# Optimization experiments

Hardware: AMD Instinct MI355X
Metric: run time of the kernel (lower is better)

Reference implementation:

```python
import jax, jax.numpy as jnp
import numpy as np
from jax.scipy.linalg import expm

DELTA = 0.01  # time step from __init__ delta
B_SZ, U_DIM, DU_DIM, H_DIM, Y_DIM = 512, 1024, 512, 2048, 1024


def setup_inputs() -> dict:
    key = jax.random.key(0)
    ks = jax.random.split(key, 6)
    inv_sqrt = lambda fan_in: 1.0 / np.sqrt(fan_in)
    u = jax.random.normal(ks[0], (B_SZ, U_DIM), jnp.float32)
    du = jax.random.normal(ks[1], (B_SZ, DU_DIM), jnp.float32)
    # torch.nn.Linear default init: U(-1/sqrt(fan_in), 1/sqrt(fan_in))
    W = jax.random.uniform(ks[2], (H_DIM, H_DIM), jnp.float32, -inv_sqrt(H_DIM), inv_sqrt(H_DIM))
    Bw = jax.random.uniform(ks[3], (H_DIM, U_DIM + DU_DIM), jnp.float32, -inv_sqrt(U_DIM + DU_DIM), inv_sqrt(U_DIM + DU_DIM))
    Cw = jax.random.uniform(ks[4], (Y_DIM, H_DIM), jnp.float32, -inv_sqrt(H_DIM), inv_sqrt(H_DIM))
    h = jax.random.normal(ks[5], (1, H_DIM), jnp.float32)
    return {"u": u, "du": du, "W": W, "Bw": Bw, "Cw": Cw, "h": h}


def reference(u, du, W, Bw, Cw, h):
    # Antisymmetric part of W
    A = 0.5 * (W - W.T)                                    # (H,H)
    A_expm = expm(A * DELTA)                               # (H,H) matrix exponential
    rec = h @ A_expm.T                                     # (1,H) recurrent term: F.linear(h, A_expm)
    A_inv = jnp.linalg.inv(A)                              # (H,H)
    # B(cat([du, u])) : (B, H)
    b = jnp.concatenate([du, u], axis=1) @ Bw.T
    # M = A^{-1} (expm(A*delta) - I); input term = M @ b^T per sample -> b @ M^T
    M = A_inv @ (A_expm - jnp.eye(H_DIM, dtype=A.dtype))   # (H,H)
    inp = b @ M.T                                          # (B,H)
    h_new = rec + inp                                      # broadcast (1,H)+(B,H) -> (B,H)
    y = h_new @ Cw.T                                       # (B,Y)
    return y
```

## Files before the change

### kernel.cpp

```cpp
#include <hip/hip_runtime.h>
#include <hip/hip_bf16.h>


#define B_SZ 512
#define U_DIM 1024
#define DU_DIM 512
#define H_DIM 2048
#define Y_DIM 1024
#define K_CAT 1536
#define DELTA_F 0.01f

typedef __hip_bfloat16 bf16;
using bf16x8f = __attribute__((ext_vector_type(8))) short;
using f32x4   = __attribute__((ext_vector_type(4))) float;

__device__ __forceinline__ short f2bs(float x) {
  union { bf16 b; short s; } u; u.b = __float2bfloat16(x); return u.s;
}
__device__ __forceinline__ int4 pack8(const float4 v0, const float4 v1) {
  union { short s[8]; int4 i; } o;
  o.s[0] = f2bs(v0.x); o.s[1] = f2bs(v0.y); o.s[2] = f2bs(v0.z); o.s[3] = f2bs(v0.w);
  o.s[4] = f2bs(v1.x); o.s[5] = f2bs(v1.y); o.s[6] = f2bs(v1.z); o.s[7] = f2bs(v1.w);
  return o.i;
}

#define LDP 72
#define LDS_SHORTS (2 * 32 * LDP + 2 * 64 * LDP)

#define NB (H_DIM * K_CAT / 8)

__global__ __launch_bounds__(256) void k1(const float* __restrict__ W, const float* __restrict__ h,
                                          const float* __restrict__ Bw, float* __restrict__ wh,
                                          float* __restrict__ wtp, short* __restrict__ Bwb) {
  const int b = blockIdx.x;
  if (b < 512) {
    const int lane = threadIdx.x & 63, wave = threadIdx.x >> 6;
    const int row = b * 4 + wave;
    const float* wr = W + (size_t)row * H_DIM;
    float s = 0.f;
#pragma unroll
    for (int it = 0; it < 8; it++) {
      int k = it * 256 + lane * 4;
      float4 a = *(const float4*)(wr + k);
      float4 hv = *(const float4*)(h + k);
      s += a.x * hv.x + a.y * hv.y + a.z * hv.z + a.w * hv.w;
    }
#pragma unroll
    for (int off = 32; off > 0; off >>= 1) s += __shfl_down(s, off);
    if (lane == 0) wh[row] = s;
  } else if (b < 768) {
    const int e = b - 512;
    const int colg = e & 7, rowg = e >> 3;
    const int k = colg * 256 + threadIdx.x;
    float s = 0.f;
    const float* base = W + (size_t)rowg * 64 * H_DIM + k;
#pragma unroll 8
    for (int i = 0; i < 64; i++) s += base[(size_t)i * H_DIM] * h[rowg * 64 + i];
    wtp[rowg * H_DIM + k] = s;
  } else {
    for (int g = (b - 768) * 256 + threadIdx.x; g < NB; g += 256 * 256) {
      int e = g * 8;
      *(int4*)(Bwb + e) = pack8(*(const float4*)(Bw + e), *(const float4*)(Bw + e + 4));
    }
  }
}

__device__ __forceinline__ void k2_tile(short* lds, float* recf, const float* __restrict__ du,
                                        const float* __restrict__ u, const short* __restrict__ B,
                                        const float* __restrict__ h, const float* __restrict__ wh,
                                        const float* __restrict__ wtp, short* __restrict__ out,
                                        int mt, int nt) {
  const int KDIM = K_CAT;
  short* As0 = lds;
  short* Bs0 = lds + 2 * 32 * LDP;
  const int tid = threadIdx.x;
  const int lane = tid & 63, wave = tid >> 6;
  const int wm = wave >> 1, wn = wave & 1;
  const int row0 = mt * 32, col0 = nt * 64;
  const int rA = tid >> 3, kc = (tid & 7) * 8;
  f32x4 acc[2] = {};
  int4 pa, pb1, pb2;
  auto ldA = [&](int kt) -> int4 {
    int col = kt * 64 + kc;
    const float* p = (col < DU_DIM) ? du + (size_t)(row0 + rA) * DU_DIM + col
                                    : u + (size_t)(row0 + rA) * U_DIM + (col - DU_DIM);
    return pack8(*(const float4*)p, *(const float4*)(p + 4));
  };
  auto ldB1 = [&](int kt) { return *(const int4*)(B + (size_t)(col0 + rA) * KDIM + kt * 64 + kc); };
  auto ldB2 = [&](int kt) { return *(const int4*)(B + (size_t)(col0 + rA + 32) * KDIM + kt * 64 + kc); };
  pa = ldA(0); pb1 = ldB1(0); pb2 = ldB2(0);
  *(int4*)&As0[rA * LDP + kc] = pa;
  *(int4*)&Bs0[rA * LDP + kc] = pb1;
  *(int4*)&Bs0[(rA + 32) * LDP + kc] = pb2;
  const int NT = KDIM / 64;
  const int kq = (lane >> 4) * 8, rm = lane & 15;
  for (int kt = 0; kt < NT; kt++) {
    const int cur = kt & 1;
    if (kt + 1 < NT) { pa = ldA(kt + 1); pb1 = ldB1(kt + 1); pb2 = ldB2(kt + 1); }
    __syncthreads();
    const short* Ac = As0 + cur * (32 * LDP);
    const short* Bc = Bs0 + cur * (64 * LDP);
    bf16x8f af[2], bfr[2][2];
#pragma unroll
    for (int ks = 0; ks < 2; ks++) {
      af[ks] = *(const bf16x8f*)&Ac[(wm * 16 + rm) * LDP + ks * 32 + kq];
#pragma unroll
      for (int j = 0; j < 2; j++)
        bfr[ks][j] = *(const bf16x8f*)&Bc[(wn * 32 + 16 * j + rm) * LDP + ks * 32 + kq];
    }
#pragma unroll
    for (int ks = 0; ks < 2; ks++)
#pragma unroll
      for (int j = 0; j < 2; j++)
        acc[j] = __builtin_amdgcn_mfma_f32_16x16x32_bf16(af[ks], bfr[ks][j], acc[j], 0, 0, 0);
    if (kt + 1 < NT) {
      short* An = As0 + (cur ^ 1) * (32 * LDP);
      short* Bn = Bs0 + (cur ^ 1) * (64 * LDP);
      *(int4*)&An[rA * LDP + kc] = pa;
      *(int4*)&Bn[rA * LDP + kc] = pb1;
      *(int4*)&Bn[(rA + 32) * LDP + kc] = pb2;
      __syncthreads();
    }
  }
  if (tid < 64) {
    int gc = col0 + tid;
    float s = 0.f;
#pragma unroll
    for (int p = 0; p < 32; p++) s += wtp[p * H_DIM + gc];
    recf[tid] = h[gc] + 0.005f * (wh[gc] - s);
  }
  __syncthreads();
  const int quad = lane >> 4;
#pragma unroll
  for (int j = 0; j < 2; j++) {
    int gc = col0 + wn * 32 + 16 * j + rm;
#pragma unroll
    for (int r = 0; r < 4; r++) {
      int gr = row0 + wm * 16 + quad * 4 + r;
      out[(size_t)gr * H_DIM + gc] = f2bs(recf[gc - col0] + DELTA_F * acc[j][r]);
    }
  }
}

__global__ __launch_bounds__(256) void k2(const float* __restrict__ du, const float* __restrict__ u,
                                          const short* __restrict__ Bwb, const float* __restrict__ h,
                                          const float* __restrict__ wh, const float* __restrict__ wtp,
                                          short* __restrict__ bb, const float* __restrict__ Cw,
                                          short* __restrict__ Cwb) {
  __shared__ __align__(16) short lds[LDS_SHORTS];
  __shared__ float recf[64];
  const int b = blockIdx.x;
  if (b < 512) {
    k2_tile(lds, recf, du, u, Bwb, h, wh, wtp, bb, b >> 5, b & 31);
  } else {
    int g = (b - 512) * 256 + threadIdx.x;
    int e = g * 8;
    *(int4*)(Cwb + e) = pack8(*(const float4*)(Cw + e), *(const float4*)(Cw + e + 4));
    e = (g + 131072) * 8;
    *(int4*)(Cwb + e) = pack8(*(const float4*)(Cw + e), *(const float4*)(Cw + e + 4));
  }
}

__global__ __launch_bounds__(256) void k3(const short* __restrict__ A, const short* __restrict__ B,
                                          float* __restrict__ y) {
  __shared__ __align__(16) short lds[LDS_SHORTS];
  const int KDIM = H_DIM;
  short* As0 = lds;
  short* Bs0 = lds + 2 * 32 * LDP;
  const int tid = threadIdx.x;
  const int lane = tid & 63, wave = tid >> 6;
  const int wm = wave >> 1, wn = wave & 1;
  const int mt = blockIdx.x >> 5, nt = blockIdx.x & 31;
  const int row0 = mt * 32, col0 = nt * 32;
  const int rA = tid >> 3, kc = (tid & 7) * 8;
  f32x4 acc = {};
  int4 pa, pb;
  auto ldA = [&](int kt) { return *(const int4*)(A + (size_t)(row0 + rA) * KDIM + kt * 64 + kc); };
  auto ldB = [&](int kt) { return *(const int4*)(B + (size_t)(col0 + rA) * KDIM + kt * 64 + kc); };
  pa = ldA(0); pb = ldB(0);
  *(int4*)&As0[rA * LDP + kc] = pa;
  *(int4*)&Bs0[rA * LDP + kc] = pb;
  const int NT = KDIM / 64;
  const int kq = (lane >> 4) * 8, rm = lane & 15;
  for (int kt = 0; kt < NT; kt++) {
    const int cur = kt & 1;
    if (kt + 1 < NT) { pa = ldA(kt + 1); pb = ldB(kt + 1); }
    __syncthreads();
    const short* Ac = As0 + cur * (32 * LDP);
    const short* Bc = Bs0 + cur * (32 * LDP);
#pragma unroll
    for (int ks = 0; ks < 2; ks++) {
      bf16x8f af = *(const bf16x8f*)&Ac[(wm * 16 + rm) * LDP + ks * 32 + kq];
      bf16x8f bf = *(const bf16x8f*)&Bc[(wn * 16 + rm) * LDP + ks * 32 + kq];
      acc = __builtin_amdgcn_mfma_f32_16x16x32_bf16(af, bf, acc, 0, 0, 0);
    }
    if (kt + 1 < NT) {
      short* An = As0 + (cur ^ 1) * (32 * LDP);
      short* Bn = Bs0 + (cur ^ 1) * (32 * LDP);
      *(int4*)&An[rA * LDP + kc] = pa;
      *(int4*)&Bn[rA * LDP + kc] = pb;
      __syncthreads();
    }
  }
  const int quad = lane >> 4;
  int gc = col0 + wn * 16 + rm;
#pragma unroll
  for (int r = 0; r < 4; r++) {
    int gr = row0 + wm * 16 + quad * 4 + r;
    y[(size_t)gr * Y_DIM + gc] = acc[r];
  }
}

extern "C" void kernel_launch(void* const* d_in, const int* in_sizes, int n_in,
                              void* d_out, int out_size, void* d_ws, size_t ws_size,
                              hipStream_t stream) {
  const float* u  = (const float*)d_in[0];
  const float* du = (const float*)d_in[1];
  const float* W  = (const float*)d_in[2];
  const float* Bw = (const float*)d_in[3];
  const float* Cw = (const float*)d_in[4];
  const float* h  = (const float*)d_in[5];
  float* y = (float*)d_out;

  char* w = (char*)d_ws;
  size_t off = 0;
  short* Bwb = (short*)(w + off); off += (size_t)H_DIM * K_CAT * sizeof(short);
  short* Cwb = (short*)(w + off); off += (size_t)Y_DIM * H_DIM * sizeof(short);
  short* bb  = (short*)(w + off); off += (size_t)B_SZ * H_DIM * sizeof(short);
  float* wh  = (float*)(w + off); off += H_DIM * sizeof(float);
  float* wtp = (float*)(w + off); off += 32 * H_DIM * sizeof(float);
  if (ws_size < off) return;

  k1<<<1024, 256, 0, stream>>>(W, h, Bw, wh, wtp, Bwb);
  k2<<<1024, 256, 0, stream>>>(du, u, Bwb, h, wh, wtp, bb, Cw, Cwb);
  k3<<<512, 256, 0, stream>>>(bb, Cwb, y);
}
```

Baseline: 122.1 us.

## Fuse second and third GEMM kernels with per-row-tile atomic flag barriers

Moves the Cw bf16 conversion into the first kernel alongside the Bw conversion and rebalances its block split. Fuses the b-projection GEMM and the output GEMM into one persistent-style kernel. Each block signals a per-row-tile counter and spins until all 32 column tiles of its 32-row slice are written, then computes its output tile. This removes one kernel launch and the global drain between the stages. In exchange it depends on all 512 blocks being co-resident (guarded by an occupancy query) and adds spin-wait and fence overhead.

```diff
diff --git a/kernel.cpp b/kernel.cpp
--- a/kernel.cpp
+++ b/kernel.cpp
@@ -26,44 +26,6 @@
 
 #define LDP 72
 #define LDS_SHORTS (2 * 32 * LDP + 2 * 64 * LDP)
-
-#define NB (H_DIM * K_CAT / 8)
-
-__global__ __launch_bounds__(256) void k1(const float* __restrict__ W, const float* __restrict__ h,
-                                          const float* __restrict__ Bw, float* __restrict__ wh,
-                                          float* __restrict__ wtp, short* __restrict__ Bwb) {
-  const int b = blockIdx.x;
-  if (b < 512) {
-    const int lane = threadIdx.x & 63, wave = threadIdx.x >> 6;
-    const int row = b * 4 + wave;
-    const float* wr = W + (size_t)row * H_DIM;
-    float s = 0.f;
-#pragma unroll
-    for (int it = 0; it < 8; it++) {
-      int k = it * 256 + lane * 4;
-      float4 a = *(const float4*)(wr + k);
-      float4 hv = *(const float4*)(h + k);
-      s += a.x * hv.x + a.y * hv.y + a.z * hv.z + a.w * hv.w;
-    }
-#pragma unroll
-    for (int off = 32; off > 0; off >>= 1) s += __shfl_down(s, off);
-    if (lane == 0) wh[row] = s;
-  } else if (b < 768) {
-    const int e = b - 512;
-    const int colg = e & 7, rowg = e >> 3;
-    const int k = colg * 256 + threadIdx.x;
-    float s = 0.f;
-    const float* base = W + (size_t)rowg * 64 * H_DIM + k;
-#pragma unroll 8
-    for (int i = 0; i < 64; i++) s += base[(size_t)i * H_DIM] * h[rowg * 64 + i];
-    wtp[rowg * H_DIM + k] = s;
-  } else {
-    for (int g = (b - 768) * 256 + threadIdx.x; g < NB; g += 256 * 256) {
-      int e = g * 8;
-      *(int4*)(Bwb + e) = pack8(*(const float4*)(Bw + e), *(const float4*)(Bw + e + 4));
-    }
-  }
-}
 
 __device__ __forceinline__ void k2_tile(short* lds, float* recf, const float* __restrict__ du,
                                         const float* __restrict__ u, const short* __restrict__ B,
@@ -142,35 +104,15 @@
   }
 }
 
-__global__ __launch_bounds__(256) void k2(const float* __restrict__ du, const float* __restrict__ u,
-                                          const short* __restrict__ Bwb, const float* __restrict__ h,
-                                          const float* __restrict__ wh, const float* __restrict__ wtp,
-                                          short* __restrict__ bb, const float* __restrict__ Cw,
-                                          short* __restrict__ Cwb) {
-  __shared__ __align__(16) short lds[LDS_SHORTS];
-  __shared__ float recf[64];
-  const int b = blockIdx.x;
-  if (b < 512) {
-    k2_tile(lds, recf, du, u, Bwb, h, wh, wtp, bb, b >> 5, b & 31);
-  } else {
-    int g = (b - 512) * 256 + threadIdx.x;
-    int e = g * 8;
-    *(int4*)(Cwb + e) = pack8(*(const float4*)(Cw + e), *(const float4*)(Cw + e + 4));
-    e = (g + 131072) * 8;
-    *(int4*)(Cwb + e) = pack8(*(const float4*)(Cw + e), *(const float4*)(Cw + e + 4));
-  }
-}
-
-__global__ __launch_bounds__(256) void k3(const short* __restrict__ A, const short* __restrict__ B,
-                                          float* __restrict__ y) {
-  __shared__ __align__(16) short lds[LDS_SHORTS];
+__device__ __forceinline__ void k3_tile(short* lds, const short* __restrict__ A,
+                                        const short* __restrict__ B, float* __restrict__ y,
+                                        int mt, int nt) {
   const int KDIM = H_DIM;
   short* As0 = lds;
   short* Bs0 = lds + 2 * 32 * LDP;
   const int tid = threadIdx.x;
   const int lane = tid & 63, wave = tid >> 6;
   const int wm = wave >> 1, wn = wave & 1;
-  const int mt = blockIdx.x >> 5, nt = blockIdx.x & 31;
   const int row0 = mt * 32, col0 = nt * 32;
   const int rA = tid >> 3, kc = (tid & 7) * 8;
   f32x4 acc = {};
@@ -211,6 +153,88 @@
   }
 }
 
+#define NB (H_DIM * K_CAT / 8)
+#define NC (Y_DIM * H_DIM / 8)
+
+__global__ __launch_bounds__(256) void k1(const float* __restrict__ W, const float* __restrict__ h,
+                                          const float* __restrict__ Bw, const float* __restrict__ Cw,
+                                          float* __restrict__ wh, float* __restrict__ wtp,
+                                          short* __restrict__ Bwb, short* __restrict__ Cwb,
+                                          int* __restrict__ flags) {
+  const int b = blockIdx.x;
+  if (b == 0 && threadIdx.x < 16) flags[threadIdx.x] = 0;
+  if (b < 256) {
+    const int lane = threadIdx.x & 63, wave = threadIdx.x >> 6;
+#pragma unroll
+    for (int i = 0; i < 2; i++) {
+      const int row = b * 8 + wave * 2 + i;
+      const float* wr = W + (size_t)row * H_DIM;
+      float s = 0.f;
+#pragma unroll
+      for (int it = 0; it < 8; it++) {
+        int k = it * 256 + lane * 4;
+        float4 a = *(const float4*)(wr + k);
+        float4 hv = *(const float4*)(h + k);
+        s += a.x * hv.x + a.y * hv.y + a.z * hv.z + a.w * hv.w;
+      }
+#pragma unroll
+      for (int off = 32; off > 0; off >>= 1) s += __shfl_down(s, off);
+      if (lane == 0) wh[row] = s;
+    }
+  } else if (b < 512) {
+    const int e = b - 256;
+    const int colg = e & 7, rowg = e >> 3;
+    const int k = colg * 256 + threadIdx.x;
+    float s = 0.f;
+    const float* base = W + (size_t)rowg * 64 * H_DIM + k;
+#pragma unroll 8
+    for (int i = 0; i < 64; i++) s += base[(size_t)i * H_DIM] * h[rowg * 64 + i];
+    wtp[rowg * H_DIM + k] = s;
+  } else {
+    for (int g = (b - 512) * 256 + threadIdx.x; g < NB + NC; g += 512 * 256) {
+      const float* src; short* dst;
+      if (g < NB) { int e = g * 8; src = Bw + e; dst = Bwb + e; }
+      else        { int e = (g - NB) * 8; src = Cw + e; dst = Cwb + e; }
+      *(int4*)dst = pack8(*(const float4*)src, *(const float4*)(src + 4));
+    }
+  }
+}
+
+__global__ void k23_fused(const float* __restrict__ du, const float* __restrict__ u,
+                          const short* __restrict__ Bwb, const float* __restrict__ h,
+                          const float* __restrict__ wh, const float* __restrict__ wtp,
+                          short* __restrict__ bb, const short* __restrict__ Cwb,
+                          float* __restrict__ y, int* __restrict__ flags) {
+  __shared__ __align__(16) short lds[LDS_SHORTS];
+  __shared__ float recf[64];
+  const int mt = blockIdx.x >> 5, nt = blockIdx.x & 31;
+  k2_tile(lds, recf, du, u, Bwb, h, wh, wtp, bb, mt, nt);
+  __threadfence();
+  __syncthreads();
+  if (threadIdx.x == 0) {
+    __hip_atomic_fetch_add(&flags[mt], 1, __ATOMIC_RELEASE, __HIP_MEMORY_SCOPE_AGENT);
+    while (__hip_atomic_load(&flags[mt], __ATOMIC_ACQUIRE, __HIP_MEMORY_SCOPE_AGENT) < 32)
+      __builtin_amdgcn_s_sleep(2);
+  }
+  __syncthreads();
+  __threadfence();
+  k3_tile(lds, bb, Cwb, y, mt, nt);
+}
+
+__global__ __launch_bounds__(256) void k2_plain(const float* __restrict__ du, const float* __restrict__ u,
+                                                const short* __restrict__ Bwb, const float* __restrict__ h,
+                                                const float* __restrict__ wh, const float* __restrict__ wtp,
+                                                short* __restrict__ bb) {
+  __shared__ __align__(16) short lds[LDS_SHORTS];
+  __shared__ float recf[64];
+  k2_tile(lds, recf, du, u, Bwb, h, wh, wtp, bb, blockIdx.x >> 5, blockIdx.x & 31);
+}
+__global__ __launch_bounds__(256) void k3_plain(const short* __restrict__ bb, const short* __restrict__ Cwb,
+                                                float* __restrict__ y) {
+  __shared__ __align__(16) short lds[LDS_SHORTS];
+  k3_tile(lds, bb, Cwb, y, blockIdx.x >> 5, blockIdx.x & 31);
+}
+
 extern "C" void kernel_launch(void* const* d_in, const int* in_sizes, int n_in,
                               void* d_out, int out_size, void* d_ws, size_t ws_size,
                               hipStream_t stream) {
@@ -229,9 +253,18 @@
   short* bb  = (short*)(w + off); off += (size_t)B_SZ * H_DIM * sizeof(short);
   float* wh  = (float*)(w + off); off += H_DIM * sizeof(float);
   float* wtp = (float*)(w + off); off += 32 * H_DIM * sizeof(float);
+  int* flags = (int*)(w + off);   off += 16 * sizeof(int);
   if (ws_size < off) return;
 
-  k1<<<1024, 256, 0, stream>>>(W, h, Bw, wh, wtp, Bwb);
-  k2<<<1024, 256, 0, stream>>>(du, u, Bwb, h, wh, wtp, bb, Cw, Cwb);
-  k3<<<512, 256, 0, stream>>>(bb, Cwb, y);
-}
+  k1<<<1024, 256, 0, stream>>>(W, h, Bw, Cw, wh, wtp, Bwb, Cwb, flags);
+
+  int occ = 0;
+  hipError_t e = hipOccupancyMaxActiveBlocksPerMultiprocessor(
+      &occ, reinterpret_cast<const void*>(&k23_fused), 256, 0);
+  if (e == hipSuccess && occ >= 2) {
+    k23_fused<<<512, 256, 0, stream>>>(du, u, Bwb, h, wh, wtp, bb, Cwb, y, flags);
+  } else {
+    k2_plain<<<512, 256, 0, stream>>>(du, u, Bwb, h, wh, wtp, bb);
+    k3_plain<<<512, 256, 0, stream>>>(bb, Cwb, y);
+  }
+}
```

Measured after the change: 232.8 us. +90.7%, slower.

## Convert weights to bf16 inside GEMM loads and split recurrent term into a rank-1 bias

Applied to the files above, without the earlier changes.

Drops the separate passes that write bf16 copies of Bw and Cw; each GEMM now reads the fp32 weights and converts them as it loads tiles. The recurrent term is no longer added to bb before the second GEMM. A small kernel computes Cw·rec once per output column, and that vector is added in the final GEMM epilogue, so bb only holds the scaled input term. The W·h reductions are interleaved with the first GEMM tiles in one launch. In exchange, the GEMMs read twice the weight bytes in fp32, and each tile converts its weights again instead of once up front.

```diff
diff --git a/kernel.cpp b/kernel.cpp
--- a/kernel.cpp
+++ b/kernel.cpp
@@ -27,49 +27,9 @@
 #define LDP 72
 #define LDS_SHORTS (2 * 32 * LDP + 2 * 64 * LDP)
 
-#define NB (H_DIM * K_CAT / 8)
-
-__global__ __launch_bounds__(256) void k1(const float* __restrict__ W, const float* __restrict__ h,
-                                          const float* __restrict__ Bw, float* __restrict__ wh,
-                                          float* __restrict__ wtp, short* __restrict__ Bwb) {
-  const int b = blockIdx.x;
-  if (b < 512) {
-    const int lane = threadIdx.x & 63, wave = threadIdx.x >> 6;
-    const int row = b * 4 + wave;
-    const float* wr = W + (size_t)row * H_DIM;
-    float s = 0.f;
-#pragma unroll
-    for (int it = 0; it < 8; it++) {
-      int k = it * 256 + lane * 4;
-      float4 a = *(const float4*)(wr + k);
-      float4 hv = *(const float4*)(h + k);
-      s += a.x * hv.x + a.y * hv.y + a.z * hv.z + a.w * hv.w;
-    }
-#pragma unroll
-    for (int off = 32; off > 0; off >>= 1) s += __shfl_down(s, off);
-    if (lane == 0) wh[row] = s;
-  } else if (b < 768) {
-    const int e = b - 512;
-    const int colg = e & 7, rowg = e >> 3;
-    const int k = colg * 256 + threadIdx.x;
-    float s = 0.f;
-    const float* base = W + (size_t)rowg * 64 * H_DIM + k;
-#pragma unroll 8
-    for (int i = 0; i < 64; i++) s += base[(size_t)i * H_DIM] * h[rowg * 64 + i];
-    wtp[rowg * H_DIM + k] = s;
-  } else {
-    for (int g = (b - 768) * 256 + threadIdx.x; g < NB; g += 256 * 256) {
-      int e = g * 8;
-      *(int4*)(Bwb + e) = pack8(*(const float4*)(Bw + e), *(const float4*)(Bw + e + 4));
-    }
-  }
-}
-
-__device__ __forceinline__ void k2_tile(short* lds, float* recf, const float* __restrict__ du,
-                                        const float* __restrict__ u, const short* __restrict__ B,
-                                        const float* __restrict__ h, const float* __restrict__ wh,
-                                        const float* __restrict__ wtp, short* __restrict__ out,
-                                        int mt, int nt) {
+__device__ __forceinline__ void bb_tile(short* lds, const float* __restrict__ du,
+                                        const float* __restrict__ u, const float* __restrict__ Bw,
+                                        short* __restrict__ bb, int mt, int nt) {
   const int KDIM = K_CAT;
   short* As0 = lds;
   short* Bs0 = lds + 2 * 32 * LDP;
@@ -86,8 +46,14 @@
                                     : u + (size_t)(row0 + rA) * U_DIM + (col - DU_DIM);
     return pack8(*(const float4*)p, *(const float4*)(p + 4));
   };
-  auto ldB1 = [&](int kt) { return *(const int4*)(B + (size_t)(col0 + rA) * KDIM + kt * 64 + kc); };
-  auto ldB2 = [&](int kt) { return *(const int4*)(B + (size_t)(col0 + rA + 32) * KDIM + kt * 64 + kc); };
+  auto ldB1 = [&](int kt) -> int4 {
+    const float* p = Bw + (size_t)(col0 + rA) * KDIM + kt * 64 + kc;
+    return pack8(*(const float4*)p, *(const float4*)(p + 4));
+  };
+  auto ldB2 = [&](int kt) -> int4 {
+    const float* p = Bw + (size_t)(col0 + rA + 32) * KDIM + kt * 64 + kc;
+    return pack8(*(const float4*)p, *(const float4*)(p + 4));
+  };
   pa = ldA(0); pb1 = ldB1(0); pb2 = ldB2(0);
   *(int4*)&As0[rA * LDP + kc] = pa;
   *(int4*)&Bs0[rA * LDP + kc] = pb1;
@@ -122,14 +88,6 @@
       __syncthreads();
     }
   }
-  if (tid < 64) {
-    int gc = col0 + tid;
-    float s = 0.f;
-#pragma unroll
-    for (int p = 0; p < 32; p++) s += wtp[p * H_DIM + gc];
-    recf[tid] = h[gc] + 0.005f * (wh[gc] - s);
-  }
-  __syncthreads();
   const int quad = lane >> 4;
 #pragma unroll
   for (int j = 0; j < 2; j++) {
@@ -137,32 +95,100 @@
 #pragma unroll
     for (int r = 0; r < 4; r++) {
       int gr = row0 + wm * 16 + quad * 4 + r;
-      out[(size_t)gr * H_DIM + gc] = f2bs(recf[gc - col0] + DELTA_F * acc[j][r]);
-    }
-  }
-}
-
-__global__ __launch_bounds__(256) void k2(const float* __restrict__ du, const float* __restrict__ u,
-                                          const short* __restrict__ Bwb, const float* __restrict__ h,
+      bb[(size_t)gr * H_DIM + gc] = f2bs(DELTA_F * acc[j][r]);
+    }
+  }
+}
+
+__global__ __launch_bounds__(256) void kA(const float* __restrict__ du, const float* __restrict__ u,
+                                          const float* __restrict__ Bw, const float* __restrict__ W,
+                                          const float* __restrict__ h, short* __restrict__ bb,
+                                          float* __restrict__ wh, float* __restrict__ wtp) {
+  __shared__ __align__(16) short lds[LDS_SHORTS];
+  const int b = blockIdx.x;
+  if ((b & 1) == 0) {
+    const int t = b >> 1;
+    bb_tile(lds, du, u, Bw, bb, t >> 5, t & 31);
+  } else {
+    const int e = b >> 1;
+    if (e < 256) {
+      const int lane = threadIdx.x & 63, wave = threadIdx.x >> 6;
+#pragma unroll
+      for (int i = 0; i < 2; i++) {
+        const int row = e * 8 + wave * 2 + i;
+        const float* wr = W + (size_t)row * H_DIM;
+        float s = 0.f;
+#pragma unroll
+        for (int it = 0; it < 8; it++) {
+          int k = it * 256 + lane * 4;
+          float4 a = *(const float4*)(wr + k);
+          float4 hv = *(const float4*)(h + k);
+          s += a.x * hv.x + a.y * hv.y + a.z * hv.z + a.w * hv.w;
+        }
+#pragma unroll
+        for (int off = 32; off > 0; off >>= 1) s += __shfl_down(s, off);
+        if (lane == 0) wh[row] = s;
+      }
+    } else {
+      const int e2 = e - 256;
+      const int colg = e2 & 7, rowg = e2 >> 3;
+      const int k = colg * 256 + threadIdx.x;
+      float s = 0.f;
+      const float* base = W + (size_t)rowg * 64 * H_DIM + k;
+#pragma unroll 8
+      for (int i = 0; i < 64; i++) s += base[(size_t)i * H_DIM] * h[rowg * 64 + i];
+      wtp[rowg * H_DIM + k] = s;
+    }
+  }
+}
+
+__global__ __launch_bounds__(256) void kB(const float* __restrict__ Cw, const float* __restrict__ h,
                                           const float* __restrict__ wh, const float* __restrict__ wtp,
-                                          short* __restrict__ bb, const float* __restrict__ Cw,
-                                          short* __restrict__ Cwb) {
-  __shared__ __align__(16) short lds[LDS_SHORTS];
-  __shared__ float recf[64];
-  const int b = blockIdx.x;
-  if (b < 512) {
-    k2_tile(lds, recf, du, u, Bwb, h, wh, wtp, bb, b >> 5, b & 31);
-  } else {
-    int g = (b - 512) * 256 + threadIdx.x;
-    int e = g * 8;
-    *(int4*)(Cwb + e) = pack8(*(const float4*)(Cw + e), *(const float4*)(Cw + e + 4));
-    e = (g + 131072) * 8;
-    *(int4*)(Cwb + e) = pack8(*(const float4*)(Cw + e), *(const float4*)(Cw + e + 4));
-  }
-}
-
-__global__ __launch_bounds__(256) void k3(const short* __restrict__ A, const short* __restrict__ B,
-                                          float* __restrict__ y) {
+                                          float* __restrict__ yrec) {
+  __shared__ float recs[H_DIM];
+  const int tid = threadIdx.x;
+  {
+    const int k0 = tid * 8;
+    float s[8] = {};
+#pragma unroll 8
+    for (int p = 0; p < 32; p++) {
+      float4 w0 = *(const float4*)(wtp + p * H_DIM + k0);
+      float4 w1 = *(const float4*)(wtp + p * H_DIM + k0 + 4);
+      s[0] += w0.x; s[1] += w0.y; s[2] += w0.z; s[3] += w0.w;
+      s[4] += w1.x; s[5] += w1.y; s[6] += w1.z; s[7] += w1.w;
+    }
+    float4 h0 = *(const float4*)(h + k0);
+    float4 h1 = *(const float4*)(h + k0 + 4);
+    float4 a0 = *(const float4*)(wh + k0);
+    float4 a1 = *(const float4*)(wh + k0 + 4);
+    recs[k0 + 0] = h0.x + 0.005f * (a0.x - s[0]);
+    recs[k0 + 1] = h0.y + 0.005f * (a0.y - s[1]);
+    recs[k0 + 2] = h0.z + 0.005f * (a0.z - s[2]);
+    recs[k0 + 3] = h0.w + 0.005f * (a0.w - s[3]);
+    recs[k0 + 4] = h1.x + 0.005f * (a1.x - s[4]);
+    recs[k0 + 5] = h1.y + 0.005f * (a1.y - s[5]);
+    recs[k0 + 6] = h1.z + 0.005f * (a1.z - s[6]);
+    recs[k0 + 7] = h1.w + 0.005f * (a1.w - s[7]);
+  }
+  __syncthreads();
+  const int lane = tid & 63, wave = tid >> 6;
+  const int row = blockIdx.x * 4 + wave;
+  const float* cr = Cw + (size_t)row * H_DIM;
+  float s = 0.f;
+#pragma unroll
+  for (int it = 0; it < 8; it++) {
+    int k = it * 256 + lane * 4;
+    float4 c = *(const float4*)(cr + k);
+    float4 r = *(const float4*)(recs + k);
+    s += c.x * r.x + c.y * r.y + c.z * r.z + c.w * r.w;
+  }
+#pragma unroll
+  for (int off = 32; off > 0; off >>= 1) s += __shfl_down(s, off);
+  if (lane == 0) yrec[row] = s;
+}
+
+__global__ __launch_bounds__(256) void kC(const short* __restrict__ bb, const float* __restrict__ Cw,
+                                          const float* __restrict__ yrec, float* __restrict__ y) {
   __shared__ __align__(16) short lds[LDS_SHORTS];
   const int KDIM = H_DIM;
   short* As0 = lds;
@@ -175,8 +201,11 @@
   const int rA = tid >> 3, kc = (tid & 7) * 8;
   f32x4 acc = {};
   int4 pa, pb;
-  auto ldA = [&](int kt) { return *(const int4*)(A + (size_t)(row0 + rA) * KDIM + kt * 64 + kc); };
-  auto ldB = [&](int kt) { return *(const int4*)(B + (size_t)(col0 + rA) * KDIM + kt * 64 + kc); };
+  auto ldA = [&](int kt) { return *(const int4*)(bb + (size_t)(row0 + rA) * KDIM + kt * 64 + kc); };
+  auto ldB = [&](int kt) -> int4 {
+    const float* p = Cw + (size_t)(col0 + rA) * KDIM + kt * 64 + kc;
+    return pack8(*(const float4*)p, *(const float4*)(p + 4));
+  };
   pa = ldA(0); pb = ldB(0);
   *(int4*)&As0[rA * LDP + kc] = pa;
   *(int4*)&Bs0[rA * LDP + kc] = pb;
@@ -207,7 +236,7 @@
 #pragma unroll
   for (int r = 0; r < 4; r++) {
     int gr = row0 + wm * 16 + quad * 4 + r;
-    y[(size_t)gr * Y_DIM + gc] = acc[r];
+    y[(size_t)gr * Y_DIM + gc] = yrec[gc] + acc[r];
   }
 }
 
@@ -224,14 +253,13 @@
 
   char* w = (char*)d_ws;
   size_t off = 0;
-  short* Bwb = (short*)(w + off); off += (size_t)H_DIM * K_CAT * sizeof(short);
-  short* Cwb = (short*)(w + off); off += (size_t)Y_DIM * H_DIM * sizeof(short);
   short* bb  = (short*)(w + off); off += (size_t)B_SZ * H_DIM * sizeof(short);
   float* wh  = (float*)(w + off); off += H_DIM * sizeof(float);
   float* wtp = (float*)(w + off); off += 32 * H_DIM * sizeof(float);
+  float* yrec= (float*)(w + off); off += Y_DIM * sizeof(float);
   if (ws_size < off) return;
 
-  k1<<<1024, 256, 0, stream>>>(W, h, Bw, wh, wtp, Bwb);
-  k2<<<1024, 256, 0, stream>>>(du, u, Bwb, h, wh, wtp, bb, Cw, Cwb);
-  k3<<<512, 256, 0, stream>>>(bb, Cwb, y);
-}
+  kA<<<1024, 256, 0, stream>>>(du, u, Bw, W, h, bb, wh, wtp);
+  kB<<<Y_DIM / 4, 256, 0, stream>>>(Cw, h, wh, wtp, yrec);
+  kC<<<512, 256, 0, stream>>>(bb, Cw, yrec, y);
+}
```

Measured after the change: 134.1 us. 9.8% more time.

## Move Cw bf16 cast into k1 and shrink k2 tiles to 32x32

Applied to the files above, without the earlier changes.

The Cw-to-bf16 conversion moves out of the second kernel into the first, alongside the W·h reductions and the Bw cast, with the reduction blocks rebalanced to handle two rows per wave. The second kernel now runs only the input GEMM, using 32x32 output tiles over 1024 blocks instead of 32x64 tiles over 512 blocks. The aim is to fill the GPU better and stop the cast blocks from competing with the GEMM. In exchange, each block reuses its A and B tiles less, A is loaded and converted twice as often, and the first kernel carries more work.

```diff
diff --git a/kernel.cpp b/kernel.cpp
--- a/kernel.cpp
+++ b/kernel.cpp
@@ -25,104 +25,107 @@
 }
 
 #define LDP 72
-#define LDS_SHORTS (2 * 32 * LDP + 2 * 64 * LDP)
+#define LDS_32x32 (4 * 32 * LDP)
 
 #define NB (H_DIM * K_CAT / 8)
+#define NC (Y_DIM * H_DIM / 8)
 
 __global__ __launch_bounds__(256) void k1(const float* __restrict__ W, const float* __restrict__ h,
-                                          const float* __restrict__ Bw, float* __restrict__ wh,
-                                          float* __restrict__ wtp, short* __restrict__ Bwb) {
+                                          const float* __restrict__ Bw, const float* __restrict__ Cw,
+                                          float* __restrict__ wh, float* __restrict__ wtp,
+                                          short* __restrict__ Bwb, short* __restrict__ Cwb) {
   const int b = blockIdx.x;
-  if (b < 512) {
-    const int lane = threadIdx.x & 63, wave = threadIdx.x >> 6;
-    const int row = b * 4 + wave;
-    const float* wr = W + (size_t)row * H_DIM;
-    float s = 0.f;
-#pragma unroll
-    for (int it = 0; it < 8; it++) {
-      int k = it * 256 + lane * 4;
-      float4 a = *(const float4*)(wr + k);
-      float4 hv = *(const float4*)(h + k);
-      s += a.x * hv.x + a.y * hv.y + a.z * hv.z + a.w * hv.w;
-    }
-#pragma unroll
-    for (int off = 32; off > 0; off >>= 1) s += __shfl_down(s, off);
-    if (lane == 0) wh[row] = s;
-  } else if (b < 768) {
-    const int e = b - 512;
+  const int tid = threadIdx.x;
+  if (b < 256) {
+    const int lane = tid & 63, wave = tid >> 6;
+#pragma unroll
+    for (int i = 0; i < 2; i++) {
+      const int row = b * 8 + wave * 2 + i;
+      const float* wr = W + (size_t)row * H_DIM;
+      float s = 0.f;
+#pragma unroll
+      for (int it = 0; it < 8; it++) {
+        int k = it * 256 + lane * 4;
+        float4 a = *(const float4*)(wr + k);
+        float4 hv = *(const float4*)(h + k);
+        s += a.x * hv.x + a.y * hv.y + a.z * hv.z + a.w * hv.w;
+      }
+#pragma unroll
+      for (int off = 32; off > 0; off >>= 1) s += __shfl_down(s, off);
+      if (lane == 0) wh[row] = s;
+    }
+  } else if (b < 512) {
+    const int e = b - 256;
     const int colg = e & 7, rowg = e >> 3;
-    const int k = colg * 256 + threadIdx.x;
+    const int k = colg * 256 + tid;
     float s = 0.f;
     const float* base = W + (size_t)rowg * 64 * H_DIM + k;
 #pragma unroll 8
     for (int i = 0; i < 64; i++) s += base[(size_t)i * H_DIM] * h[rowg * 64 + i];
     wtp[rowg * H_DIM + k] = s;
-  } else {
-    for (int g = (b - 768) * 256 + threadIdx.x; g < NB; g += 256 * 256) {
+  } else if (b < 768) {
+    for (int g = (b - 512) * 256 + tid; g < NB; g += 256 * 256) {
       int e = g * 8;
       *(int4*)(Bwb + e) = pack8(*(const float4*)(Bw + e), *(const float4*)(Bw + e + 4));
     }
-  }
-}
-
-__device__ __forceinline__ void k2_tile(short* lds, float* recf, const float* __restrict__ du,
-                                        const float* __restrict__ u, const short* __restrict__ B,
-                                        const float* __restrict__ h, const float* __restrict__ wh,
-                                        const float* __restrict__ wtp, short* __restrict__ out,
-                                        int mt, int nt) {
+  } else {
+    for (int g = (b - 768) * 256 + tid; g < NC; g += 256 * 256) {
+      int e = g * 8;
+      *(int4*)(Cwb + e) = pack8(*(const float4*)(Cw + e), *(const float4*)(Cw + e + 4));
+    }
+  }
+}
+
+__global__ __launch_bounds__(256) void k2(const float* __restrict__ du, const float* __restrict__ u,
+                                          const short* __restrict__ Bwb, const float* __restrict__ h,
+                                          const float* __restrict__ wh, const float* __restrict__ wtp,
+                                          short* __restrict__ bb) {
+  __shared__ __align__(16) short lds[LDS_32x32];
+  __shared__ float recf[32];
   const int KDIM = K_CAT;
   short* As0 = lds;
   short* Bs0 = lds + 2 * 32 * LDP;
   const int tid = threadIdx.x;
   const int lane = tid & 63, wave = tid >> 6;
   const int wm = wave >> 1, wn = wave & 1;
-  const int row0 = mt * 32, col0 = nt * 64;
+  const int mt = blockIdx.x >> 6, nt = blockIdx.x & 63;
+  const int row0 = mt * 32, col0 = nt * 32;
   const int rA = tid >> 3, kc = (tid & 7) * 8;
-  f32x4 acc[2] = {};
-  int4 pa, pb1, pb2;
+  f32x4 acc = {};
+  int4 pa, pb;
   auto ldA = [&](int kt) -> int4 {
     int col = kt * 64 + kc;
     const float* p = (col < DU_DIM) ? du + (size_t)(row0 + rA) * DU_DIM + col
                                     : u + (size_t)(row0 + rA) * U_DIM + (col - DU_DIM);
     return pack8(*(const float4*)p, *(const float4*)(p + 4));
   };
-  auto ldB1 = [&](int kt) { return *(const int4*)(B + (size_t)(col0 + rA) * KDIM + kt * 64 + kc); };
-  auto ldB2 = [&](int kt) { return *(const int4*)(B + (size_t)(col0 + rA + 32) * KDIM + kt * 64 + kc); };
-  pa = ldA(0); pb1 = ldB1(0); pb2 = ldB2(0);
+  auto ldB = [&](int kt) { return *(const int4*)(Bwb + (size_t)(col0 + rA) * KDIM + kt * 64 + kc); };
+  pa = ldA(0); pb = ldB(0);
   *(int4*)&As0[rA * LDP + kc] = pa;
-  *(int4*)&Bs0[rA * LDP + kc] = pb1;
-  *(int4*)&Bs0[(rA + 32) * LDP + kc] = pb2;
+  *(int4*)&Bs0[rA * LDP + kc] = pb;
   const int NT = KDIM / 64;
   const int kq = (lane >> 4) * 8, rm = lane & 15;
   for (int kt = 0; kt < NT; kt++) {
     const int cur = kt & 1;
-    if (kt + 1 < NT) { pa = ldA(kt + 1); pb1 = ldB1(kt + 1); pb2 = ldB2(kt + 1); }
+    if (kt + 1 < NT) { pa = ldA(kt + 1); pb = ldB(kt + 1); }
     __syncthreads();
     const short* Ac = As0 + cur * (32 * LDP);
-    const short* Bc = Bs0 + cur * (64 * LDP);
-    bf16x8f af[2], bfr[2][2];
+    const short* Bc = Bs0 + cur * (32 * LDP);
 #pragma unroll
     for (int ks = 0; ks < 2; ks++) {
-      af[ks] = *(const bf16x8f*)&Ac[(wm * 16 + rm) * LDP + ks * 32 + kq];
-#pragma unroll
-      for (int j = 0; j < 2; j++)
-        bfr[ks][j] = *(const bf16x8f*)&Bc[(wn * 32 + 16 * j + rm) * LDP + ks * 32 + kq];
-    }
-#pragma unroll
-    for (int ks = 0; ks < 2; ks++)
-#pragma unroll
-      for (int j = 0; j < 2; j++)
-        acc[j] = __builtin_amdgcn_mfma_f32_16x16x32_bf16(af[ks], bfr[ks][j], acc[j], 0, 0, 0);
+      bf16x8f af = *(const bf16x8f*)&Ac[(wm * 16 + rm) * LDP + ks * 32 + kq];
+      bf16x8f bf = *(const bf16x8f*)&Bc[(wn * 16 + rm) * LDP + ks * 32 + kq];
+      acc = __builtin_amdgcn_mfma_f32_16x16x32_bf16(af, bf, acc, 0, 0, 0);
+    }
     if (kt + 1 < NT) {
       short* An = As0 + (cur ^ 1) * (32 * LDP);
-      short* Bn = Bs0 + (cur ^ 1) * (64 * LDP);
+      short* Bn = Bs0 + (cur ^ 1) * (32 * LDP);
       *(int4*)&An[rA * LDP + kc] = pa;
-      *(int4*)&Bn[rA * LDP + kc] = pb1;
-      *(int4*)&Bn[(rA + 32) * LDP + kc] = pb2;
+      *(int4*)&Bn[rA * LDP + kc] = pb;
       __syncthreads();
     }
   }
-  if (tid < 64) {
+  if (tid < 32) {
     int gc = col0 + tid;
     float s = 0.f;
 #pragma unroll
@@ -131,39 +134,17 @@
   }
   __syncthreads();
   const int quad = lane >> 4;
-#pragma unroll
-  for (int j = 0; j < 2; j++) {
-    int gc = col0 + wn * 32 + 16 * j + rm;
-#pragma unroll
-    for (int r = 0; r < 4; r++) {
-      int gr = row0 + wm * 16 + quad * 4 + r;
-      out[(size_t)gr * H_DIM + gc] = f2bs(recf[gc - col0] + DELTA_F * acc[j][r]);
-    }
-  }
-}
-
-__global__ __launch_bounds__(256) void k2(const float* __restrict__ du, const float* __restrict__ u,
-                                          const short* __restrict__ Bwb, const float* __restrict__ h,
-                                          const float* __restrict__ wh, const float* __restrict__ wtp,
-                                          short* __restrict__ bb, const float* __restrict__ Cw,
-                                          short* __restrict__ Cwb) {
-  __shared__ __align__(16) short lds[LDS_SHORTS];
-  __shared__ float recf[64];
-  const int b = blockIdx.x;
-  if (b < 512) {
-    k2_tile(lds, recf, du, u, Bwb, h, wh, wtp, bb, b >> 5, b & 31);
-  } else {
-    int g = (b - 512) * 256 + threadIdx.x;
-    int e = g * 8;
-    *(int4*)(Cwb + e) = pack8(*(const float4*)(Cw + e), *(const float4*)(Cw + e + 4));
-    e = (g + 131072) * 8;
-    *(int4*)(Cwb + e) = pack8(*(const float4*)(Cw + e), *(const float4*)(Cw + e + 4));
+  int gc = col0 + wn * 16 + rm;
+#pragma unroll
+  for (int r = 0; r < 4; r++) {
+    int gr = row0 + wm * 16 + quad * 4 + r;
+    bb[(size_t)gr * H_DIM + gc] = f2bs(recf[gc - col0] + DELTA_F * acc[r]);
   }
 }
 
 __global__ __launch_bounds__(256) void k3(const short* __restrict__ A, const short* __restrict__ B,
                                           float* __restrict__ y) {
-  __shared__ __align__(16) short lds[LDS_SHORTS];
+  __shared__ __align__(16) short lds[LDS_32x32];
   const int KDIM = H_DIM;
   short* As0 = lds;
   short* Bs0 = lds + 2 * 32 * LDP;
@@ -231,7 +212,7 @@
   float* wtp = (float*)(w + off); off += 32 * H_DIM * sizeof(float);
   if (ws_size < off) return;
 
-  k1<<<1024, 256, 0, stream>>>(W, h, Bw, wh, wtp, Bwb);
-  k2<<<1024, 256, 0, stream>>>(du, u, Bwb, h, wh, wtp, bb, Cw, Cwb);
+  k1<<<1024, 256, 0, stream>>>(W, h, Bw, Cw, wh, wtp, Bwb, Cwb);
+  k2<<<1024, 256, 0, stream>>>(du, u, Bwb, h, wh, wtp, bb);
   k3<<<512, 256, 0, stream>>>(bb, Cwb, y);
 }
```

Result: no change. 123.4 us (+1.1%).
